# Kernel tuning notes

Hardware: AMD Instinct MI355X
Metric: run time of the kernel (lower is better)

## Reference

```python
import jax, jax.numpy as jnp
import numpy as np

D_MODEL = 1024
NUM_HEADS = 16
HEAD_DIM = D_MODEL // NUM_HEADS
B, S = 4, 2048


def setup_inputs() -> dict:
    key = jax.random.key(0)
    ks = jax.random.split(key, 11)
    sc = 1.0 / np.sqrt(D_MODEL)
    return {
        "query": jax.random.normal(ks[0], (B, S, D_MODEL), jnp.float32),
        "key": jax.random.normal(ks[1], (B, S, D_MODEL), jnp.float32),
        "value": jax.random.normal(ks[2], (B, S, D_MODEL), jnp.float32),
        "Wq": jax.random.normal(ks[3], (D_MODEL, D_MODEL), jnp.float32) * sc,
        "bq": jnp.zeros((D_MODEL,), jnp.float32),
        "Wk": jax.random.normal(ks[4], (D_MODEL, D_MODEL), jnp.float32) * sc,
        "bk": jnp.zeros((D_MODEL,), jnp.float32),
        "Wv": jax.random.normal(ks[5], (D_MODEL, D_MODEL), jnp.float32) * sc,
        "bv": jnp.zeros((D_MODEL,), jnp.float32),
        "Wo": jax.random.normal(ks[6], (D_MODEL, D_MODEL), jnp.float32) * sc,
        "bo": jnp.zeros((D_MODEL,), jnp.float32),
    }


def _split_heads(x):
    b, s, _ = x.shape
    return x.reshape(b, s, NUM_HEADS, HEAD_DIM).transpose(0, 2, 1, 3)  # [B,H,S,Dh]


def reference(query, key, value, Wq, bq, Wk, bk, Wv, bv, Wo, bo):
    q = _split_heads(query @ Wq + bq)
    k = _split_heads(key @ Wk + bk)
    v = _split_heads(value @ Wv + bv)
    scores = jnp.einsum("bhqd,bhkd->bhqk", q, k) / np.sqrt(HEAD_DIM)
    attn = jax.nn.softmax(scores, axis=-1)
    out = jnp.einsum("bhqk,bhkd->bhqd", attn, v)
    out = out.transpose(0, 2, 1, 3).reshape(query.shape[0], -1, D_MODEL)
    return out @ Wo + bo
```

## Files before the change

### kernel.cpp

```cpp
#include <hip/hip_runtime.h>

typedef unsigned short u16;
typedef unsigned int   u32;
typedef unsigned long long u64;
typedef __attribute__((ext_vector_type(8))) short bf16x8;
typedef __attribute__((ext_vector_type(4))) float f32x4;

#define S_  2048
#define DH  64
#define DM  1024
#define BS  8192
#define CS  0.18033688011112042f

static __device__ __forceinline__ float bf2f(u16 v){ return __uint_as_float(((u32)v)<<16); }
static __device__ __forceinline__ u16 f2bf(float f){
  u32 x = __float_as_uint(f);
  return (u16)((x + 0x7fffu + ((x>>16)&1u)) >> 16);
}
#if __has_builtin(__builtin_amdgcn_cvt_pk_bf16_f32)
static __device__ __forceinline__ u32 pk2(float x, float y){
  typedef __attribute__((ext_vector_type(2))) __bf16 bf2v;
  union { bf2v v; u32 u; } c; c.v = __builtin_amdgcn_cvt_pk_bf16_f32(x, y); return c.u;
}
#else
static __device__ __forceinline__ u32 pk2(float x, float y){
  return (u32)f2bf(x) | ((u32)f2bf(y) << 16);
}
#endif
#if __has_builtin(__builtin_amdgcn_exp2f)
#define EXP2F(x) __builtin_amdgcn_exp2f(x)
#else
#define EXP2F(x) exp2f(x)
#endif

static __device__ __forceinline__ void dma16(const u16* g, const u16* l){
  __builtin_amdgcn_global_load_lds(
      (const __attribute__((address_space(1))) u32*)(u64)(uintptr_t)g,
      (__attribute__((address_space(3))) u32*)(u32)(u64)(uintptr_t)l, 16, 0, 0);
}

static __device__ __forceinline__ bf16x8 lds_frag(const u16* p){
  union { bf16x8 f; uint2 u[2]; } w;
  w.u[0] = *(const uint2*)(p);
  w.u[1] = *(const uint2*)(p+4);
  return w.f;
}
static __device__ __forceinline__ bf16x8 frag16v(const u16* p){
  union { bf16x8 f; uint4 u; } w;
  w.u = *(const uint4*)p;
  return w.f;
}
static __device__ __forceinline__ void stage16_bf(const u16* __restrict__ g, u16* s){
  uint4 a = *(const uint4*)g;
  uint4 b = *(const uint4*)(g+8);
  *(uint2*)(s+0)  = make_uint2(a.x,a.y);
  *(uint2*)(s+4)  = make_uint2(a.z,a.w);
  *(uint2*)(s+8)  = make_uint2(b.x,b.y);
  *(uint2*)(s+12) = make_uint2(b.z,b.w);
}
static __device__ __forceinline__ void stage16_f32(const float* __restrict__ g, u16* s){
  float4 a0 = ((const float4*)g)[0];
  float4 a1 = ((const float4*)g)[1];
  float4 a2 = ((const float4*)g)[2];
  float4 a3 = ((const float4*)g)[3];
  *(uint2*)(s+0)  = make_uint2(pk2(a0.x,a0.y), pk2(a0.z,a0.w));
  *(uint2*)(s+4)  = make_uint2(pk2(a1.x,a1.y), pk2(a1.z,a1.w));
  *(uint2*)(s+8)  = make_uint2(pk2(a2.x,a2.y), pk2(a2.z,a2.w));
  *(uint2*)(s+12) = make_uint2(pk2(a3.x,a3.y), pk2(a3.z,a3.w));
}

__global__ __launch_bounds__(256) void detect_f32(const u16* __restrict__ q, int* flag){
  __shared__ int cnt[256];
  int tid = threadIdx.x;
  int bad = 0;
  for (int i = tid; i < 8192; i += 256){
    u32 e = (q[i] >> 7) & 0xFFu;
    bad += (e == 0xFFu) || (e == 0u);
  }
  cnt[tid] = bad;
  __syncthreads();
  for (int s = 128; s > 0; s >>= 1){ if (tid < s) cnt[tid] += cnt[tid+s]; __syncthreads(); }
  if (tid == 0) flag[0] = (cnt[0] > 0) ? 1 : 0;
}

__global__ __launch_bounds__(256) void transpose4(const void* __restrict__ i0,
    const void* __restrict__ i1, const void* __restrict__ i2, const void* __restrict__ i3,
    u16* o0, u16* o1, u16* o2, u16* o3, const int* __restrict__ flag){
  __shared__ u16 tile[32][33];
  int z = blockIdx.z;
  const void* in = z==0?i0 : z==1?i1 : z==2?i2 : i3;
  u16* out = z==0?o0 : z==1?o1 : z==2?o2 : o3;
  bool f32 = flag[0] != 0;
  int tx = threadIdx.x, ty = threadIdx.y;
  int c  = blockIdx.x*32 + tx;
  int r0 = blockIdx.y*32;
  for (int i=ty;i<32;i+=8){
    long off = (long)(r0+i)*DM + c;
    tile[i][tx] = f32 ? f2bf(((const float*)in)[off]) : ((const u16*)in)[off];
  }
  __syncthreads();
  int rr = r0 + tx, c0 = blockIdx.x*32;
  for (int i=ty;i<32;i+=8) out[(long)(c0+i)*DM + rr] = tile[tx][i];
}

__global__ __launch_bounds__(256) void convert3(const void* __restrict__ a0,
    const void* __restrict__ a1, const void* __restrict__ a2,
    u16* o0, u16* o1, u16* o2, const int* __restrict__ flag){
  int z = blockIdx.z;
  const void* in = z==0?a0 : z==1?a1 : a2;
  u16* out = z==0?o0 : z==1?o1 : o2;
  long i = ((long)blockIdx.x*256 + threadIdx.x)*8;
  if (flag[0]){
    const float4* p = (const float4*)((const float*)in + i);
    float4 x = p[0], y = p[1];
    *(uint4*)(out + i) = make_uint4(pk2(x.x,x.y), pk2(x.z,x.w), pk2(y.x,y.y), pk2(y.z,y.w));
  } else {
    *(uint4*)(out + i) = *(const uint4*)((const u16*)in + i);
  }
}

template<int ADMA>
__global__ __launch_bounds__(256) void gemm_qkv(
    const void* __restrict__ A0, const void* __restrict__ A1, const void* __restrict__ A2,
    const u16* __restrict__ W0, const u16* __restrict__ W1, const u16* __restrict__ W2,
    const void* __restrict__ bv0, const void* __restrict__ bv1, const void* __restrict__ bv2,
    u16* C0, u16* C1, u16* C2, const int* __restrict__ flag){
  constexpr int AST = ADMA ? 32 : 36;
  __shared__ __align__(16) u16 As[128*AST];
  __shared__ __align__(16) u16 Bs[128*32];
  int z = blockIdx.z;
  const void* A  = z==0?A0 : z==1?A1 : A2;
  const u16* BT  = z==0?W0 : z==1?W1 : W2;
  const void* bias = z==0?bv0 : z==1?bv1 : bv2;
  u16* C = z==0?C0 : z==1?C1 : C2;
  const int f = flag[0];
  const bool aF32 = (!ADMA) && (f != 0);
  const bool bF32 = (f != 0);
  int tid = threadIdx.x;
  int by = blockIdx.x, bx = blockIdx.y;
  int lane = tid & 63, w = tid >> 6;
  int t = lane & 15, q = lane >> 4;
  int wr = w >> 1, wc = w & 1;
  f32x4 acc[4][4];
  #pragma unroll
  for(int i=0;i<4;i++) for(int j=0;j<4;j++) for(int k=0;k<4;k++) acc[i][j][k]=0.f;

  const u16* gB = BT + ((long)(bx*128 + w*32 + (lane>>2))*DM + (lane&3)*8);
  const u16* lB = &Bs[(w*32)*32];
  const u16* gA_dma = nullptr; const u16* lA_dma = nullptr;
  long aoff = 0;
  if constexpr (ADMA){
    gA_dma = (const u16*)A + ((long)(by*128 + w*32 + (lane>>2))*DM + (lane&3)*8);
    lA_dma = &As[(w*32)*32];
  } else {
    aoff = (long)(by*128 + (tid>>1))*DM + (tid&1)*16;
  }
  const u16* ArdB = &As[(wr*64 + t)*AST + q*8];
  const u16* BrdB = &Bs[(wc*64 + t)*32  + q*8];

  for (int k0=0; k0<DM; k0+=32){
    dma16(gB + k0, lB);
    dma16(gB + 16*DM + k0, lB + 16*32);
    if constexpr (ADMA){
      dma16(gA_dma + k0, lA_dma);
      dma16(gA_dma + 16*DM + k0, lA_dma + 16*32);
    } else {
      u16* AsW = &As[(tid>>1)*36 + (tid&1)*16];
      if (aF32) stage16_f32((const float*)A + aoff + k0, AsW);
      else      stage16_bf ((const u16*)A  + aoff + k0, AsW);
    }
    __syncthreads();
    bf16x8 af[4], bfr[4];
    #pragma unroll
    for (int rt=0;rt<4;rt++) af[rt]  = lds_frag(ArdB + rt*16*AST);
    #pragma unroll
    for (int ct=0;ct<4;ct++) bfr[ct] = lds_frag(BrdB + ct*16*32);
    #pragma unroll
    for (int rt=0;rt<4;rt++)
      #pragma unroll
      for (int ct=0;ct<4;ct++)
        acc[rt][ct] = __builtin_amdgcn_mfma_f32_16x16x32_bf16(af[rt], bfr[ct], acc[rt][ct], 0,0,0);
    __syncthreads();
  }
  float scale = (z==0) ? CS : 1.0f;
  #pragma unroll
  for (int ct=0;ct<4;ct++){
    int col = bx*128 + wc*64 + ct*16 + t;
    float bvv = bF32 ? ((const float*)bias)[col] : bf2f(((const u16*)bias)[col]);
    #pragma unroll
    for (int rt=0;rt<4;rt++){
      int row0 = by*128 + wr*64 + rt*16 + q*4;
      if (z == 2){
        int bb = row0 >> 11, s = row0 & 2047;
        long vbase = (long)bb*2097152 + (long)col*2048
                   + (s & ~63) + ((s & 15) << 2) + ((s >> 4) & 3);
        #pragma unroll
        for (int r=0;r<4;r++)
          C[vbase + r*4] = f2bf(acc[rt][ct][r] + bvv);
      } else {
        #pragma unroll
        for (int r=0;r<4;r++)
          C[(long)(row0+r)*DM + col] = f2bf((acc[rt][ct][r] + bvv)*scale);
      }
    }
  }
}

__global__ __launch_bounds__(256) void gemm_o(const u16* __restrict__ A,
    const u16* __restrict__ BT, const void* __restrict__ bias, void* __restrict__ C,
    const int* __restrict__ flag){
  __shared__ __align__(16) u16 As[128*32];
  __shared__ __align__(16) u16 Bs[128*32];
  const int f = flag[0];
  int tid = threadIdx.x;
  int by = blockIdx.x, bx = blockIdx.y;
  int lane = tid & 63, w = tid >> 6;
  int t = lane & 15, q = lane >> 4;
  int wr = w >> 1, wc = w & 1;
  f32x4 acc[4][4];
  #pragma unroll
  for(int i=0;i<4;i++) for(int j=0;j<4;j++) for(int k=0;k<4;k++) acc[i][j][k]=0.f;

  const u16* gA = A  + ((long)(by*128 + w*32 + (lane>>2))*DM + (lane&3)*8);
  const u16* gB = BT + ((long)(bx*128 + w*32 + (lane>>2))*DM + (lane&3)*8);
  const u16* lA = &As[(w*32)*32];
  const u16* lB = &Bs[(w*32)*32];
  const u16* ArdB = &As[(wr*64 + t)*32 + q*8];
  const u16* BrdB = &Bs[(wc*64 + t)*32 + q*8];

  for (int k0=0; k0<DM; k0+=32){
    dma16(gA + k0, lA);
    dma16(gA + 16*DM + k0, lA + 16*32);
    dma16(gB + k0, lB);
    dma16(gB + 16*DM + k0, lB + 16*32);
    __syncthreads();
    bf16x8 af[4], bfr[4];
    #pragma unroll
    for (int rt=0;rt<4;rt++) af[rt]  = lds_frag(ArdB + rt*16*32);
    #pragma unroll
    for (int ct=0;ct<4;ct++) bfr[ct] = lds_frag(BrdB + ct*16*32);
    #pragma unroll
    for (int rt=0;rt<4;rt++)
      #pragma unroll
      for (int ct=0;ct<4;ct++)
        acc[rt][ct] = __builtin_amdgcn_mfma_f32_16x16x32_bf16(af[rt], bfr[ct], acc[rt][ct], 0,0,0);
    __syncthreads();
  }
  #pragma unroll
  for (int ct=0;ct<4;ct++){
    int col = bx*128 + wc*64 + ct*16 + t;
    float bvv = f ? ((const float*)bias)[col] : bf2f(((const u16*)bias)[col]);
    #pragma unroll
    for (int rt=0;rt<4;rt++){
      int row0 = by*128 + wr*64 + rt*16 + q*4;
      #pragma unroll
      for (int r=0;r<4;r++){
        long idx = (long)(row0+r)*DM + col;
        float v = acc[rt][ct][r] + bvv;
        if (f) ((float*)C)[idx] = v;
        else   ((u16*)C)[idx]  = f2bf(v);
      }
    }
  }
}

__global__ __launch_bounds__(256,3) void attn4(const u16* __restrict__ Q,
    const u16* __restrict__ Kb, const u16* __restrict__ Vt, u16* __restrict__ O){
  __shared__ __align__(16) u16 Ks[2][4096];
  __shared__ __align__(16) u16 Vs[2][4096];
  __shared__ __align__(16) u16 Ps[4][2304];
  int tid = threadIdx.x;
  int qt = blockIdx.x, bh = blockIdx.y;
  int b = bh >> 4, h = bh & 15;
  int lane = tid & 63, w = tid >> 6;
  int t = lane & 15, q = lane >> 4;

  const u16* Qbase = Q + ((long)(b*S_ + qt*128 + w*32 + t)*DM + h*DH + q*8);
  bf16x8 qf[2][2];
  qf[0][0] = frag16v(Qbase);
  qf[0][1] = frag16v(Qbase + 32);
  qf[1][0] = frag16v(Qbase + 16*DM);
  qf[1][1] = frag16v(Qbase + 16*DM + 32);

  int r0 = tid >> 3;
  int cb = ((tid & 7) * 16) ^ ((r0 & 7) << 4);
  const char* gK = (const char*)Kb + (((long)(b*S_ + r0)*DM + h*DH) << 1) + cb;
  const char* gV = (const char*)Vt + ((((long)bh << 17) + ((long)r0 << 11)) << 1) + cb;
  const long gK1 = ((long)32*DM) << 1;
  const long gV1 = ((long)32*S_) << 1;
  const int ld0 = w*512, ld1 = 2048 + w*512;

  f32x4 o[2][4];
  #pragma unroll
  for (int i=0;i<2;i++) for (int j=0;j<4;j++) for (int k=0;k<4;k++) o[i][j][k]=0.f;
  f32x4 lsum[2];
  #pragma unroll
  for (int i=0;i<2;i++) for (int k=0;k<4;k++) lsum[i][k]=0.f;

  const int xorv = (t & 7) << 4;

  dma16((const u16*)(gK),       &Ks[0][ld0]);
  dma16((const u16*)(gK + gK1), &Ks[0][ld1]);
  dma16((const u16*)(gV),       &Vs[0][ld0]);
  dma16((const u16*)(gV + gV1), &Vs[0][ld1]);

  for (int kt=0; kt<32; kt++){
    int cur = kt & 1;
    if (kt < 31){
      long ko = ((long)(kt+1)*64*DM) << 1;
      long vo = (long)(kt+1) << 7;
      dma16((const u16*)(gK + ko),       &Ks[cur^1][ld0]);
      dma16((const u16*)(gK + ko + gK1), &Ks[cur^1][ld1]);
      dma16((const u16*)(gV + vo),       &Vs[cur^1][ld0]);
      dma16((const u16*)(gV + vo + gV1), &Vs[cur^1][ld1]);
      asm volatile("s_waitcnt vmcnt(4)" ::: "memory");
    } else {
      asm volatile("s_waitcnt vmcnt(0)" ::: "memory");
    }
    __builtin_amdgcn_s_barrier();

    const u16* Kc = Ks[cur];
    const u16* Vc = Vs[cur];

    f32x4 sacc[2][4];
    #pragma unroll
    for (int i=0;i<2;i++) for (int j=0;j<4;j++) for (int k=0;k<4;k++) sacc[i][j][k]=0.f;
    #pragma unroll
    for (int ks=0; ks<2; ks++){
      int off = ((ks*64 + q*16) ^ xorv) >> 1;
      bf16x8 k0 = frag16v(Kc + (t     )*64 + off);
      bf16x8 k1 = frag16v(Kc + (16 + t)*64 + off);
      bf16x8 k2 = frag16v(Kc + (32 + t)*64 + off);
      bf16x8 k3 = frag16v(Kc + (48 + t)*64 + off);
      #pragma unroll
      for (int rt=0; rt<2; rt++){
        sacc[rt][0] = __builtin_amdgcn_mfma_f32_16x16x32_bf16(qf[rt][ks], k0, sacc[rt][0],0,0,0);
        sacc[rt][1] = __builtin_amdgcn_mfma_f32_16x16x32_bf16(qf[rt][ks], k1, sacc[rt][1],0,0,0);
        sacc[rt][2] = __builtin_amdgcn_mfma_f32_16x16x32_bf16(qf[rt][ks], k2, sacc[rt][2],0,0,0);
        sacc[rt][3] = __builtin_amdgcn_mfma_f32_16x16x32_bf16(qf[rt][ks], k3, sacc[rt][3],0,0,0);
      }
    }

    #pragma unroll
    for (int rt=0; rt<2; rt++){
      #pragma unroll
      for (int r=0; r<4; r++){
        float p0 = EXP2F(sacc[rt][0][r]);
        float p1 = EXP2F(sacc[rt][1][r]);
        float p2 = EXP2F(sacc[rt][2][r]);
        float p3 = EXP2F(sacc[rt][3][r]);
        lsum[rt][r] += (p0+p1)+(p2+p3);
        *(uint2*)&Ps[w][(rt*16 + q*4 + r)*72 + t*4] = make_uint2(pk2(p0,p1), pk2(p2,p3));
      }
    }

    #pragma unroll
    for (int ks=0; ks<2; ks++){
      int off = ((ks*64 + q*16) ^ xorv) >> 1;
      bf16x8 v0 = frag16v(Vc + (t     )*64 + off);
      bf16x8 v1 = frag16v(Vc + (16 + t)*64 + off);
      bf16x8 v2 = frag16v(Vc + (32 + t)*64 + off);
      bf16x8 v3 = frag16v(Vc + (48 + t)*64 + off);
      #pragma unroll
      for (int rt=0; rt<2; rt++){
        bf16x8 pf = frag16v(&Ps[w][(rt*16 + t)*72 + ks*32 + q*8]);
        o[rt][0] = __builtin_amdgcn_mfma_f32_16x16x32_bf16(pf, v0, o[rt][0],0,0,0);
        o[rt][1] = __builtin_amdgcn_mfma_f32_16x16x32_bf16(pf, v1, o[rt][1],0,0,0);
        o[rt][2] = __builtin_amdgcn_mfma_f32_16x16x32_bf16(pf, v2, o[rt][2],0,0,0);
        o[rt][3] = __builtin_amdgcn_mfma_f32_16x16x32_bf16(pf, v3, o[rt][3],0,0,0);
      }
    }
    __builtin_amdgcn_s_barrier();
  }

  #pragma unroll
  for (int rt=0; rt<2; rt++){
    #pragma unroll
    for (int r=0; r<4; r++){
      float l = lsum[rt][r];
      l += __shfl_xor(l, 1);
      l += __shfl_xor(l, 2);
      l += __shfl_xor(l, 4);
      l += __shfl_xor(l, 8);
      float inv = 1.f / l;
      int row = qt*128 + w*32 + rt*16 + q*4 + r;
      #pragma unroll
      for (int ct=0; ct<4; ct++)
        O[(long)(b*S_ + row)*DM + h*DH + ct*16 + t] = f2bf(o[rt][ct][r] * inv);
    }
  }
}

extern "C" void kernel_launch(void* const* d_in, const int* in_sizes, int n_in,
                              void* d_out, int out_size, void* d_ws, size_t ws_size,
                              hipStream_t stream){
  (void)in_sizes; (void)n_in; (void)out_size;
  const void* xq = d_in[0];
  const void* xk = d_in[1];
  const void* xv = d_in[2];
  const void* Wq = d_in[3];
  const void* bq = d_in[4];
  const void* Wk = d_in[5];
  const void* bk = d_in[6];
  const void* Wv = d_in[7];
  const void* bv = d_in[8];
  const void* Wo = d_in[9];
  const void* bo = d_in[10];

  int* flag = (int*)d_ws;
  u16* base = (u16*)((char*)d_ws + 256);
  const long NT = (long)BS*DM;
  u16* Qb  = base;
  u16* Kbf = base + NT;
  u16* Vt  = base + 2*NT;
  u16* WqT = base + 3*NT;
  u16* WkT = WqT + (long)DM*DM;
  u16* WvT = WkT + (long)DM*DM;
  u16* WoT = WvT + (long)DM*DM;
  u16* Xc0 = WoT + (long)DM*DM;
  u16* Xc1 = Xc0 + NT;
  u16* Xc2 = Xc1 + NT;
  size_t need_pre = 256 + (size_t)(6*NT + 4*(long)DM*DM)*2;
  bool pre = ws_size >= need_pre;

  detect_f32<<<1, 256, 0, stream>>>((const u16*)xq, flag);

  transpose4<<<dim3(32,32,4), dim3(32,8,1), 0, stream>>>(Wq, Wk, Wv, Wo,
      WqT, WkT, WvT, WoT, flag);

  dim3 gb(256,1,1);
  if (pre){
    convert3<<<dim3(4096,1,3), gb, 0, stream>>>(xq, xk, xv, Xc0, Xc1, Xc2, flag);
    gemm_qkv<1><<<dim3(64,8,3), gb, 0, stream>>>(Xc0, Xc1, Xc2,
        WqT, WkT, WvT, bq, bk, bv, Qb, Kbf, Vt, flag);
  } else {
    gemm_qkv<0><<<dim3(64,8,3), gb, 0, stream>>>(xq, xk, xv,
        WqT, WkT, WvT, bq, bk, bv, Qb, Kbf, Vt, flag);
  }

  attn4<<<dim3(16,64,1), gb, 0, stream>>>(Qb, Kbf, Vt, Qb );

  gemm_o<<<dim3(64,8,1), gb, 0, stream>>>(Qb, WoT, bo, d_out, flag);
}
```

Baseline: 388.7 us.

## Keep softmax probabilities in registers via transposed QK MFMA, drop LDS P buffer

Attention now computes S^T by swapping MFMA operands so the exp'd scores land directly in the A-fragment layout for the PV MFMA, which removes the per-wave LDS staging buffer and its round trip. The row sum comes from an extra MFMA against a ones vector rather than a shuffle reduction. The V store in the QKV GEMM is reordered to match and packed into 8-byte writes. The kernel also adds s_setprio around the MFMA blocks, raises the occupancy hint to 4, and remaps blocks so each batch/head is swizzled across the grid. The cost is one extra MFMA per PV step and higher register pressure under the tighter occupancy bound.

```diff
diff --git a/kernel.cpp b/kernel.cpp
--- a/kernel.cpp
+++ b/kernel.cpp
@@ -193,10 +193,10 @@
       if (z == 2){
         int bb = row0 >> 11, s = row0 & 2047;
         long vbase = (long)bb*2097152 + (long)col*2048
-                   + (s & ~63) + ((s & 15) << 2) + ((s >> 4) & 3);
-        #pragma unroll
-        for (int r=0;r<4;r++)
-          C[vbase + r*4] = f2bf(acc[rt][ct][r] + bvv);
+                   + (s & ~63) + ((rt>>1)<<5) + (q<<3) + ((rt&1)<<2);
+        u32 lo = pk2(acc[rt][ct][0]+bvv, acc[rt][ct][1]+bvv);
+        u32 hi = pk2(acc[rt][ct][2]+bvv, acc[rt][ct][3]+bvv);
+        *(uint2*)(C + vbase) = make_uint2(lo,hi);
       } else {
         #pragma unroll
         for (int r=0;r<4;r++)
@@ -264,13 +264,15 @@
   }
 }
 
-__global__ __launch_bounds__(256,3) void attn4(const u16* __restrict__ Q,
+__global__ __launch_bounds__(256,4) void attn5(const u16* __restrict__ Q,
     const u16* __restrict__ Kb, const u16* __restrict__ Vt, u16* __restrict__ O){
   __shared__ __align__(16) u16 Ks[2][4096];
   __shared__ __align__(16) u16 Vs[2][4096];
-  __shared__ __align__(16) u16 Ps[4][2304];
   int tid = threadIdx.x;
-  int qt = blockIdx.x, bh = blockIdx.y;
+  int bid = blockIdx.x;
+  int qt = bid >> 6;
+  int s6 = bid & 63;
+  int bh = (s6 & 7)*8 + (s6 >> 3);
   int b = bh >> 4, h = bh & 15;
   int lane = tid & 63, w = tid >> 6;
   int t = lane & 15, q = lane >> 4;
@@ -293,9 +295,13 @@
   f32x4 o[2][4];
   #pragma unroll
   for (int i=0;i<2;i++) for (int j=0;j<4;j++) for (int k=0;k<4;k++) o[i][j][k]=0.f;
-  f32x4 lsum[2];
-  #pragma unroll
-  for (int i=0;i<2;i++) for (int k=0;k<4;k++) lsum[i][k]=0.f;
+  f32x4 o4[2];
+  #pragma unroll
+  for (int i=0;i<2;i++) for (int k=0;k<4;k++) o4[i][k]=0.f;
+
+  union { bf16x8 f; u32 u[4]; } vone;
+  { u32 ovv = (t==0) ? 0x3F803F80u : 0u;
+    vone.u[0]=ovv; vone.u[1]=ovv; vone.u[2]=ovv; vone.u[3]=ovv; }
 
   const int xorv = (t & 7) << 4;
 
@@ -332,25 +338,31 @@
       bf16x8 k1 = frag16v(Kc + (16 + t)*64 + off);
       bf16x8 k2 = frag16v(Kc + (32 + t)*64 + off);
       bf16x8 k3 = frag16v(Kc + (48 + t)*64 + off);
+      __builtin_amdgcn_s_setprio(1);
       #pragma unroll
       for (int rt=0; rt<2; rt++){
-        sacc[rt][0] = __builtin_amdgcn_mfma_f32_16x16x32_bf16(qf[rt][ks], k0, sacc[rt][0],0,0,0);
-        sacc[rt][1] = __builtin_amdgcn_mfma_f32_16x16x32_bf16(qf[rt][ks], k1, sacc[rt][1],0,0,0);
-        sacc[rt][2] = __builtin_amdgcn_mfma_f32_16x16x32_bf16(qf[rt][ks], k2, sacc[rt][2],0,0,0);
-        sacc[rt][3] = __builtin_amdgcn_mfma_f32_16x16x32_bf16(qf[rt][ks], k3, sacc[rt][3],0,0,0);
+        sacc[rt][0] = __builtin_amdgcn_mfma_f32_16x16x32_bf16(k0, qf[rt][ks], sacc[rt][0],0,0,0);
+        sacc[rt][1] = __builtin_amdgcn_mfma_f32_16x16x32_bf16(k1, qf[rt][ks], sacc[rt][1],0,0,0);
+        sacc[rt][2] = __builtin_amdgcn_mfma_f32_16x16x32_bf16(k2, qf[rt][ks], sacc[rt][2],0,0,0);
+        sacc[rt][3] = __builtin_amdgcn_mfma_f32_16x16x32_bf16(k3, qf[rt][ks], sacc[rt][3],0,0,0);
       }
-    }
-
+      __builtin_amdgcn_s_setprio(0);
+    }
+
+    union { bf16x8 f; u32 u[4]; } af[2][2];
     #pragma unroll
     for (int rt=0; rt<2; rt++){
-      #pragma unroll
-      for (int r=0; r<4; r++){
-        float p0 = EXP2F(sacc[rt][0][r]);
-        float p1 = EXP2F(sacc[rt][1][r]);
-        float p2 = EXP2F(sacc[rt][2][r]);
-        float p3 = EXP2F(sacc[rt][3][r]);
-        lsum[rt][r] += (p0+p1)+(p2+p3);
-        *(uint2*)&Ps[w][(rt*16 + q*4 + r)*72 + t*4] = make_uint2(pk2(p0,p1), pk2(p2,p3));
+      float ev[4][4];
+      #pragma unroll
+      for (int c=0; c<4; c++)
+        #pragma unroll
+        for (int r=0; r<4; r++) ev[c][r] = EXP2F(sacc[rt][c][r]);
+      #pragma unroll
+      for (int ks=0; ks<2; ks++){
+        af[rt][ks].u[0] = pk2(ev[2*ks  ][0], ev[2*ks  ][1]);
+        af[rt][ks].u[1] = pk2(ev[2*ks  ][2], ev[2*ks  ][3]);
+        af[rt][ks].u[2] = pk2(ev[2*ks+1][0], ev[2*ks+1][1]);
+        af[rt][ks].u[3] = pk2(ev[2*ks+1][2], ev[2*ks+1][3]);
       }
     }
 
@@ -361,14 +373,16 @@
       bf16x8 v1 = frag16v(Vc + (16 + t)*64 + off);
       bf16x8 v2 = frag16v(Vc + (32 + t)*64 + off);
       bf16x8 v3 = frag16v(Vc + (48 + t)*64 + off);
+      __builtin_amdgcn_s_setprio(1);
       #pragma unroll
       for (int rt=0; rt<2; rt++){
-        bf16x8 pf = frag16v(&Ps[w][(rt*16 + t)*72 + ks*32 + q*8]);
-        o[rt][0] = __builtin_amdgcn_mfma_f32_16x16x32_bf16(pf, v0, o[rt][0],0,0,0);
-        o[rt][1] = __builtin_amdgcn_mfma_f32_16x16x32_bf16(pf, v1, o[rt][1],0,0,0);
-        o[rt][2] = __builtin_amdgcn_mfma_f32_16x16x32_bf16(pf, v2, o[rt][2],0,0,0);
-        o[rt][3] = __builtin_amdgcn_mfma_f32_16x16x32_bf16(pf, v3, o[rt][3],0,0,0);
+        o[rt][0] = __builtin_amdgcn_mfma_f32_16x16x32_bf16(af[rt][ks].f, v0, o[rt][0],0,0,0);
+        o[rt][1] = __builtin_amdgcn_mfma_f32_16x16x32_bf16(af[rt][ks].f, v1, o[rt][1],0,0,0);
+        o[rt][2] = __builtin_amdgcn_mfma_f32_16x16x32_bf16(af[rt][ks].f, v2, o[rt][2],0,0,0);
+        o[rt][3] = __builtin_amdgcn_mfma_f32_16x16x32_bf16(af[rt][ks].f, v3, o[rt][3],0,0,0);
+        o4[rt]   = __builtin_amdgcn_mfma_f32_16x16x32_bf16(af[rt][ks].f, vone.f, o4[rt],0,0,0);
       }
+      __builtin_amdgcn_s_setprio(0);
     }
     __builtin_amdgcn_s_barrier();
   }
@@ -377,11 +391,7 @@
   for (int rt=0; rt<2; rt++){
     #pragma unroll
     for (int r=0; r<4; r++){
-      float l = lsum[rt][r];
-      l += __shfl_xor(l, 1);
-      l += __shfl_xor(l, 2);
-      l += __shfl_xor(l, 4);
-      l += __shfl_xor(l, 8);
+      float l = __shfl(o4[rt][r], lane & 48);
       float inv = 1.f / l;
       int row = qt*128 + w*32 + rt*16 + q*4 + r;
       #pragma unroll
@@ -438,7 +448,7 @@
         WqT, WkT, WvT, bq, bk, bv, Qb, Kbf, Vt, flag);
   }
 
-  attn4<<<dim3(16,64,1), gb, 0, stream>>>(Qb, Kbf, Vt, Qb );
+  attn5<<<dim3(1024,1,1), gb, 0, stream>>>(Qb, Kbf, Vt, Qb );
 
   gemm_o<<<dim3(64,8,1), gb, 0, stream>>>(Qb, WoT, bo, d_out, flag);
 }
```

New measurement: 360.5 us. 1.08x faster.
